# Kernel optimization log

Hardware: AMD Instinct MI355X
Metric: run time of the kernel (lower is better)

The kernel has to match this reference:

```python
import jax, jax.numpy as jnp
import numpy as np
from jax import lax

B, L, E, P, K, KS, H, T = 64, 512, 256, 64, 512, 3, 512, 53
V, MAXL = 50000, 512


def _span_idx(k):
    ks, kl = jax.random.split(k)
    starts = jax.random.randint(ks, (B,), 1, L - 9)
    spans = jax.random.randint(kl, (B,), 0, 8)
    return jnp.stack([starts, starts + spans], axis=1)  # [B,2], 1<=s<=e<L-1


def setup_inputs() -> dict:
    key = jax.random.key(0)
    ks = jax.random.split(key, 12)
    context = jax.random.randint(ks[0], (B, L), 0, V)
    subject_idx = _span_idx(ks[1])
    object_idx = _span_idx(ks[2])
    subject_dis = jax.random.randint(ks[3], (B, L), 0, 2 * MAXL)
    object_dis = jax.random.randint(ks[4], (B, L), 0, 2 * MAXL)
    embed_table = jax.random.normal(ks[5], (V, E), jnp.float32) * 0.02
    pos_table = jax.random.normal(ks[6], (2 * MAXL, P), jnp.float32) * 0.02
    Cin = 3 * E + 2 * P
    conv_w = jax.random.normal(ks[7], (K, Cin, KS), jnp.float32) * 0.02
    conv_b = jnp.zeros((K,), jnp.float32)
    lin1_w = jax.random.normal(ks[8], (H, K), jnp.float32) * 0.02
    lin1_b = jnp.zeros((H,), jnp.float32)
    lin2_w = jax.random.normal(ks[9], (T, 6 * E + H), jnp.float32) * 0.02
    lin2_b = jnp.zeros((T,), jnp.float32)
    return {"context": context, "subject_idx": subject_idx, "object_idx": object_idx,
            "subject_dis": subject_dis, "object_dis": object_dis,
            "embed_table": embed_table, "pos_table": pos_table,
            "conv_w": conv_w, "conv_b": conv_b,
            "lin1_w": lin1_w, "lin1_b": lin1_b, "lin2_w": lin2_w, "lin2_b": lin2_b}


def _entity_features(embed, idx):
    # embed: [B,L,E'], idx: [B,2] (start,end) inclusive span
    s, e = idx[:, 0], idx[:, 1]
    pos = jnp.arange(L)
    mask = (pos[None, :] >= s[:, None]) & (pos[None, :] <= e[:, None])  # [B,L]
    cnt = mask.sum(axis=1).astype(embed.dtype)[:, None]
    mean = jnp.einsum('ble,bl->be', embed, mask.astype(embed.dtype)) / cnt
    bidx = jnp.arange(embed.shape[0])
    left = embed[bidx, s - 1]                       # start>=1 always in data (torch: start>=0 branch)
    right_ok = (e + 1) < L
    right = jnp.where(right_ok[:, None], embed[bidx, jnp.clip(e + 1, 0, L - 1)], 0.0)
    return jnp.concatenate([mean, left, right], axis=1)  # [B,3E']


def reference(context, subject_idx, object_idx, subject_dis, object_dis,
              embed_table, pos_table, conv_w, conv_b,
              lin1_w, lin1_b, lin2_w, lin2_b):
    embed = embed_table[context]                    # [B,L,E]
    subj = _entity_features(embed, subject_idx)     # [B,3E]
    obj = _entity_features(embed, object_idx)       # [B,3E]

    # shift-and-concat window features (zero pad one step each side)
    epad = jnp.pad(embed, ((0, 0), (1, 1), (0, 0)))
    word = jnp.concatenate([epad[:, :-2], epad[:, 1:-1], epad[:, 2:]], axis=2)  # [B,L,3E]

    pos_feat = jnp.concatenate([pos_table[subject_dis], pos_table[object_dis]], axis=2)  # [B,L,2P]
    sent = jnp.concatenate([word, pos_feat], axis=2).transpose(0, 2, 1)  # [B,C,L]

    conv = lax.conv_general_dilated(sent, conv_w, window_strides=(1,),
                                    padding=[(KS // 2, KS // 2)],
                                    dimension_numbers=('NCH', 'OIH', 'NCH'))
    conv = conv + conv_b[None, :, None]             # [B,K,L]
    pooled = conv.max(axis=2)                       # global maxpool -> [B,K]
    sent_h = jnp.tanh(pooled @ lin1_w.T + lin1_b)   # [B,H]

    com = jnp.concatenate([subj, obj, sent_h], axis=1)  # [B,6E+H]
    scores = com @ lin2_w.T + lin2_b                # [B,T]; decode = argmax(scores, 1)
    return scores
```

## Files before the change

kernel.cpp:

```cpp
#include <hip/hip_runtime.h>
#include <hip/hip_bf16.h>
#include <hip/hip_fp8.h>
#include <stdint.h>

#define B_   64
#define L_   512
#define E_   256
#define P_   64
#define KOUT 512
#define KS_  3
#define H_   512
#define T_   53
#define CINW 2688
#define LE   516
#define LPP  514
#define COMW 2048

#define FP8_S    64.0f
#define DESCALE  (1.0f / 4096.0f)

#define SEC_CW    0
#define SEC_EMBP  512
#define SEC_POSP  (SEC_EMBP + (B_ * LE / 4))
#define SEC_ENT   (SEC_POSP + (B_ * LPP / 4))
#define SEC_POOL  (SEC_ENT + 2 * B_)
#define SEC_END   (SEC_POOL + 32)

typedef __attribute__((ext_vector_type(4))) float f32x4;
typedef __attribute__((ext_vector_type(4))) int   i32x4;
typedef __attribute__((ext_vector_type(8))) int   i32x8;

__device__ __forceinline__ unsigned enc_f(float x) {
    unsigned u = __float_as_uint(x);
    return (u & 0x80000000u) ? ~u : (u | 0x80000000u);
}
__device__ __forceinline__ float dec_f(unsigned e) {
    return __uint_as_float((e & 0x80000000u) ? (e & 0x7fffffffu) : ~e);
}
__device__ __forceinline__ unsigned char f8c(float x) {
    __hip_fp8_e4m3 t(x);
    return t.__x;
}

__device__ __forceinline__ void cp16(const void* g, void* l) {
    __builtin_amdgcn_global_load_lds(
        (const __attribute__((address_space(1))) unsigned int*)g,
        (__attribute__((address_space(3))) unsigned int*)l,
        16, 0, 0);
}

__global__ void prep(const float* __restrict__ conv_w,
                     const int* __restrict__ context,
                     const int* __restrict__ sidx,
                     const int* __restrict__ oidx,
                     const int* __restrict__ sdis,
                     const int* __restrict__ odis,
                     const float* __restrict__ etab,
                     const float* __restrict__ ptab,
                     unsigned char* __restrict__ wce,
                     unsigned char* __restrict__ wcp,
                     __hip_bfloat16* __restrict__ wcorr,
                     unsigned char* __restrict__ embp,
                     unsigned char* __restrict__ posp,
                     float* __restrict__ com,
                     unsigned* __restrict__ pooled) {
    __shared__ float w[CINW];
    const int blk = blockIdx.x;
    const int tid = threadIdx.x;

    if (blk < SEC_EMBP) {
        int n = blk;
        const float* src = conv_w + (size_t)n * CINW;
        for (int i = tid; i < CINW; i += 256) w[i] = src[i];
        __syncthreads();
        for (int i = tid; i < 5 * E_; i += 256) {
            int d = i >> 8, c = i & 255;
            float s = 0.f;
#pragma unroll
            for (int tau = 0; tau <= 2; tau++) {
                int seg = d - tau;
                if (seg >= 0 && seg <= 2) s += w[(seg * 256 + c) * 3 + tau];
            }
            wce[((size_t)d * KOUT + n) * E_ + c] = f8c(s * FP8_S);
        }
        for (int i = tid; i < 3 * 128; i += 256) {
            int tau = i >> 7, p = i & 127;
            wcp[((size_t)tau * KOUT + n) * 128 + p] = f8c(w[(768 + p) * 3 + tau] * FP8_S);
        }
        for (int i = tid; i < 2 * E_; i += 256) {
            int which = i >> 8, c = i & 255;
            wcorr[((size_t)which * KOUT + n) * E_ + c] =
                __float2bfloat16(which ? w[c * 3 + 2] : w[(512 + c) * 3 + 0]);
        }
    } else if (blk < SEC_POSP) {
        int row = (blk - SEC_EMBP) * 4 + (tid >> 6);
        int lane = tid & 63;
        int b = row / LE, r = row % LE;
        unsigned char* out = embp + (size_t)row * E_;
        if (r < 2 || r >= LE - 2) {
            *(uchar4*)(out + lane * 4) = (uchar4){0, 0, 0, 0};
            return;
        }
        int token = context[b * L_ + (r - 2)];
        float4 v = *(const float4*)(etab + (size_t)token * E_ + lane * 4);
        uchar4 pk;
        pk.x = f8c(v.x * FP8_S); pk.y = f8c(v.y * FP8_S);
        pk.z = f8c(v.z * FP8_S); pk.w = f8c(v.w * FP8_S);
        *(uchar4*)(out + lane * 4) = pk;
    } else if (blk < SEC_ENT) {
        int row = (blk - SEC_POSP) * 4 + (tid >> 6);
        int lane = tid & 63;
        int b = row / LPP, r = row % LPP;
        unsigned char* out = posp + (size_t)row * 128;
        if (r < 1 || r >= LPP - 1) {
            *(unsigned short*)(out + lane * 2) = 0;
            return;
        }
        int l = r - 1;
        int which = lane >> 5;
        int i2 = (lane & 31) * 2;
        int t = which ? odis[b * L_ + l] : sdis[b * L_ + l];
        float2 v = *(const float2*)(ptab + (size_t)t * P_ + i2);
        unsigned short pk = (unsigned short)f8c(v.x * FP8_S)
                          | ((unsigned short)f8c(v.y * FP8_S) << 8);
        *(unsigned short*)(out + which * 64 + i2) = pk;
    } else if (blk < SEC_POOL) {
        int idx = blk - SEC_ENT;
        int b = idx >> 1, which = idx & 1;
        const int* sp = which ? oidx : sidx;
        int s = sp[b * 2 + 0], e = sp[b * 2 + 1];
        const int* ctx = context + b * L_;
        float* outb = com + (size_t)b * COMW + which * 768;
        int d = tid;
        float sum = 0.f;
        for (int x = s; x <= e; ++x) sum += etab[(size_t)ctx[x] * E_ + d];
        outb[d] = sum / (float)(e - s + 1);
        outb[256 + d] = etab[(size_t)ctx[s - 1] * E_ + d];
        float r = 0.f;
        if (e + 1 < L_) r = etab[(size_t)ctx[e + 1] * E_ + d];
        outb[512 + d] = r;
    } else {
        int base = ((blk - SEC_POOL) * 256 + tid) * 4;
        *(uint4*)(pooled + base) = (uint4){0, 0, 0, 0};
    }
}

__global__ void corr_k(const int* __restrict__ ctx,
                       const float* __restrict__ etab,
                       const __hip_bfloat16* __restrict__ wcorr,
                       float* __restrict__ corr) {
    int wid = blockIdx.x * 4 + (threadIdx.x >> 6);
    int lane = threadIdx.x & 63;
    int n4    = wid & 127;
    int which = (wid >> 7) & 1;
    int b     = wid >> 8;
    int token = ctx[b * L_ + (which ? L_ - 1 : 0)];
    float4 ev = *(const float4*)(etab + (size_t)token * E_ + lane * 4);
#pragma unroll
    for (int k = 0; k < 4; k++) {
        int n = n4 * 4 + k;
        const __hip_bfloat16* wr = wcorr + ((size_t)which * KOUT + n) * E_ + lane * 4;
        float s = ev.x * __bfloat162float(wr[0]) + ev.y * __bfloat162float(wr[1])
                + ev.z * __bfloat162float(wr[2]) + ev.w * __bfloat162float(wr[3]);
#pragma unroll
        for (int off = 32; off > 0; off >>= 1) s += __shfl_down(s, off, 64);
        if (lane == 0) corr[(b * 2 + which) * KOUT + n] = s;
    }
}

__global__ void __launch_bounds__(256, 2)
conv_gemm_pool(const unsigned char* __restrict__ embp,
               const unsigned char* __restrict__ posp,
               const unsigned char* __restrict__ wce,
               const unsigned char* __restrict__ wcp,
               const float* __restrict__ corr,
               unsigned* __restrict__ pooled) {
    __shared__ unsigned char sT[2][2][128 * 128];

    const int tid  = threadIdx.x;
    const int lane = tid & 63;
    const int wave = tid >> 6;
    const int mt = blockIdx.x;
    const int nt = blockIdx.y;
    const int b  = mt >> 2;
    const int l0 = (mt & 3) * 128;
    const int n0 = nt * 128;

    const int wr = (wave & 1) * 64;
    const int wc = (wave >> 1) * 64;
    const int m  = lane & 15;
    const int q  = lane >> 4;

    f32x4 acc[4][4];
#pragma unroll
    for (int i = 0; i < 4; i++)
#pragma unroll
        for (int j = 0; j < 4; j++) acc[i][j] = (f32x4){0.f, 0.f, 0.f, 0.f};

    const int srow = tid >> 3;
    const int ssw  = ((tid & 7) ^ (srow & 7)) << 4;

    auto bases = [&](int t, const char*& A, int& As, const char*& Bx, int& Bs) {
        if (t < 10) {
            int tap = t >> 1, kc = (t & 1) << 7;
            A  = (const char*)embp + ((size_t)(b * LE + l0 + tap) << 8) + kc;
            As = E_;
            Bx = (const char*)wce + ((size_t)(tap * KOUT + n0) << 8) + kc;
            Bs = E_;
        } else {
            int tap = t - 10;
            A  = (const char*)posp + ((size_t)(b * LPP + l0 + tap) << 7);
            As = 128;
            Bx = (const char*)wcp + ((size_t)(tap * KOUT + n0) << 7);
            Bs = 128;
        }
    };

    auto stage = [&](int bf_, const char* A, int As, const char* Bx, int Bs) {
        char* dA = (char*)&sT[bf_][0][0] + tid * 16;
        char* dB = (char*)&sT[bf_][1][0] + tid * 16;
#pragma unroll
        for (int rnd = 0; rnd < 4; rnd++) {
            int r = srow + rnd * 32;
            cp16(A  + r * As + ssw, dA + rnd * 4096);
            cp16(Bx + r * Bs + ssw, dB + rnd * 4096);
        }
    };

    auto frag = [&](const unsigned char* base, int row) -> i32x8 {
        const unsigned char* rp = base + row * 128;
        int x  = (row & 7) << 4;
        i32x4 lo = *(const i32x4*)(rp + (((q << 1) << 4) ^ x));
        i32x4 hi = *(const i32x4*)(rp + ((((q << 1) | 1) << 4) ^ x));
        return (i32x8){lo[0], lo[1], lo[2], lo[3], hi[0], hi[1], hi[2], hi[3]};
    };

    auto compute = [&](int bf_) {
        const unsigned char* pA = &sT[bf_][0][0];
        const unsigned char* pB = &sT[bf_][1][0];
        i32x8 af[4];
#pragma unroll
        for (int i = 0; i < 4; i++) af[i] = frag(pA, wr + i * 16 + m);
#pragma unroll
        for (int j = 0; j < 4; j++) {
            i32x8 bfv = frag(pB, wc + j * 16 + m);
#pragma unroll
            for (int i = 0; i < 4; i++)
                acc[i][j] = __builtin_amdgcn_mfma_scale_f32_16x16x128_f8f6f4(
                    af[i], bfv, acc[i][j], 0, 0, 0, 0x7f7f7f7f, 0, 0x7f7f7f7f);
        }
    };

    {
        const char *A0, *B0; int As0, Bs0;
        bases(0, A0, As0, B0, Bs0);
        stage(0, A0, As0, B0, Bs0);
    }
    int cur = 0;
#pragma unroll 1
    for (int t = 0; t < 13; t++) {
        if (t < 12) {
            const char *A1, *B1; int As1, Bs1;
            bases(t + 1, A1, As1, B1, Bs1);
            stage(cur ^ 1, A1, As1, B1, Bs1);
            asm volatile("s_waitcnt vmcnt(8)" ::: "memory");
        } else {
            asm volatile("s_waitcnt vmcnt(0)" ::: "memory");
        }
        __builtin_amdgcn_s_barrier();
        __builtin_amdgcn_sched_barrier(0);
        compute(cur);
        __builtin_amdgcn_sched_barrier(0);
        __builtin_amdgcn_s_barrier();
        cur ^= 1;
    }

    const float* corrb = corr + b * 2 * KOUT;
#pragma unroll
    for (int j = 0; j < 4; j++) {
        int col = n0 + wc + j * 16 + m;
        float mx = -3.4e38f;
#pragma unroll
        for (int i = 0; i < 4; i++)
#pragma unroll
            for (int r = 0; r < 4; r++) {
                float v = acc[i][j][r] * DESCALE;
                int l = l0 + wr + i * 16 + q * 4 + r;
                if (l == 0)      v -= corrb[col];
                if (l == L_ - 1) v -= corrb[KOUT + col];
                mx = fmaxf(mx, v);
            }
        mx = fmaxf(mx, __shfl_xor(mx, 16, 64));
        mx = fmaxf(mx, __shfl_xor(mx, 32, 64));
        if (q == 0) atomicMax(&pooled[b * KOUT + col], enc_f(mx));
    }
}

__global__ void lin1_k(const unsigned* __restrict__ pooled,
                       const float* __restrict__ conv_b,
                       const float* __restrict__ lin1_w,
                       const float* __restrict__ lin1_b,
                       float* __restrict__ com) {
    int bid = blockIdx.x;
    int wave = threadIdx.x >> 6, lane = threadIdx.x & 63;
    int b = bid >> 7;
    int h = (bid & 127) * 4 + wave;
    const float* w = lin1_w + (size_t)h * KOUT;
    const unsigned* pb = pooled + b * KOUT;
    float s = 0.f;
#pragma unroll
    for (int i = 0; i < 8; i++) {
        int k = lane + 64 * i;
        s += (dec_f(pb[k]) + conv_b[k]) * w[k];
    }
#pragma unroll
    for (int off = 32; off > 0; off >>= 1) s += __shfl_down(s, off, 64);
    if (lane == 0) com[(size_t)b * COMW + 1536 + h] = tanhf(s + lin1_b[h]);
}

__global__ void lin2_k(const float* __restrict__ com,
                       const float* __restrict__ lin2_w,
                       const float* __restrict__ lin2_b,
                       float* __restrict__ out) {
    int b = blockIdx.x;
    int wave = threadIdx.x >> 6, lane = threadIdx.x & 63;
    int t = blockIdx.y * 4 + wave;
    if (t >= T_) return;
    const float* w = lin2_w + (size_t)t * COMW;
    const float* c = com + (size_t)b * COMW;
    float s = 0.f;
#pragma unroll
    for (int i = 0; i < 32; i++) {
        int k = lane + 64 * i;
        s += c[k] * w[k];
    }
#pragma unroll
    for (int off = 32; off > 0; off >>= 1) s += __shfl_down(s, off, 64);
    if (lane == 0) out[b * T_ + t] = s + lin2_b[t];
}

extern "C" void kernel_launch(void* const* d_in, const int* in_sizes, int n_in,
                              void* d_out, int out_size, void* d_ws, size_t ws_size,
                              hipStream_t stream) {
    const int*   context = (const int*)d_in[0];
    const int*   sidx    = (const int*)d_in[1];
    const int*   oidx    = (const int*)d_in[2];
    const int*   sdis    = (const int*)d_in[3];
    const int*   odis    = (const int*)d_in[4];
    const float* etab    = (const float*)d_in[5];
    const float* ptab    = (const float*)d_in[6];
    const float* conv_w  = (const float*)d_in[7];
    const float* conv_b  = (const float*)d_in[8];
    const float* lin1_w  = (const float*)d_in[9];
    const float* lin1_b  = (const float*)d_in[10];
    const float* lin2_w  = (const float*)d_in[11];
    const float* lin2_b  = (const float*)d_in[12];
    float* out = (float*)d_out;

    char* ws = (char*)d_ws;
    size_t off = 0;
    unsigned char* embp = (unsigned char*)(ws + off);
    off += (size_t)B_ * LE * E_;
    off = (off + 255) & ~(size_t)255;
    unsigned char* posp = (unsigned char*)(ws + off);
    off += (size_t)B_ * LPP * 128;
    off = (off + 255) & ~(size_t)255;
    unsigned char* wce = (unsigned char*)(ws + off);
    off += (size_t)5 * KOUT * E_;
    off = (off + 255) & ~(size_t)255;
    unsigned char* wcp = (unsigned char*)(ws + off);
    off += (size_t)3 * KOUT * 128;
    off = (off + 255) & ~(size_t)255;
    __hip_bfloat16* wcorr = (__hip_bfloat16*)(ws + off);
    off += (size_t)2 * KOUT * E_ * 2;
    off = (off + 255) & ~(size_t)255;
    float* corr = (float*)(ws + off);
    off += (size_t)B_ * 2 * KOUT * 4;
    off = (off + 255) & ~(size_t)255;
    unsigned* pooled = (unsigned*)(ws + off);
    off += (size_t)B_ * KOUT * 4;
    off = (off + 255) & ~(size_t)255;
    float* com = (float*)(ws + off);
    off += (size_t)B_ * COMW * 4;

    prep<<<dim3(SEC_END), dim3(256), 0, stream>>>(
        conv_w, context, sidx, oidx, sdis, odis, etab, ptab,
        wce, wcp, wcorr, embp, posp, com, pooled);
    corr_k<<<dim3(4096), dim3(256), 0, stream>>>(context, etab, wcorr, corr);
    conv_gemm_pool<<<dim3(256, 4), dim3(256), 0, stream>>>(embp, posp, wce, wcp, corr, pooled);
    lin1_k<<<dim3(8192), dim3(256), 0, stream>>>(pooled, conv_b, lin1_w, lin1_b, com);
    lin2_k<<<dim3(B_, 14), dim3(256), 0, stream>>>(com, lin2_w, lin2_b, out);
}
```

Baseline: 181.4 us.

## Reuse one A window across conv taps and fold corr into prep

```diff
diff --git a/kernel.cpp b/kernel.cpp
--- a/kernel.cpp
+++ b/kernel.cpp
@@ -59,9 +59,9 @@
                      const float* __restrict__ ptab,
                      unsigned char* __restrict__ wce,
                      unsigned char* __restrict__ wcp,
-                     __hip_bfloat16* __restrict__ wcorr,
                      unsigned char* __restrict__ embp,
                      unsigned char* __restrict__ posp,
+                     float* __restrict__ corr,
                      float* __restrict__ com,
                      unsigned* __restrict__ pooled) {
     __shared__ float w[CINW];
@@ -87,10 +87,22 @@
             int tau = i >> 7, p = i & 127;
             wcp[((size_t)tau * KOUT + n) * 128 + p] = f8c(w[(768 + p) * 3 + tau] * FP8_S);
         }
-        for (int i = tid; i < 2 * E_; i += 256) {
-            int which = i >> 8, c = i & 255;
-            wcorr[((size_t)which * KOUT + n) * E_ + c] =
-                __float2bfloat16(which ? w[c * 3 + 2] : w[(512 + c) * 3 + 0]);
+        {
+            int p   = tid >> 1, sub = tid & 1;
+            int bb  = p >> 1, which = p & 1;
+            int token = context[bb * L_ + (which ? L_ - 1 : 0)];
+            const float4* er4 = (const float4*)(etab + (size_t)token * E_ + sub * 128);
+            int A = which ? (sub * 384 + 2) : (1536 + sub * 384);
+            float s = 0.f;
+#pragma unroll 8
+            for (int c4 = 0; c4 < 32; c4++) {
+                float4 v = er4[c4];
+                int c = c4 * 4;
+                s += v.x * w[A + 3 * c]     + v.y * w[A + 3 * c + 3]
+                   + v.z * w[A + 3 * c + 6] + v.w * w[A + 3 * c + 9];
+            }
+            s += __shfl_xor(s, 1, 64);
+            if (sub == 0) corr[(bb * 2 + which) * KOUT + n] = s;
         }
     } else if (blk < SEC_POSP) {
         int row = (blk - SEC_EMBP) * 4 + (tid >> 6);
@@ -145,37 +157,15 @@
     }
 }
 
-__global__ void corr_k(const int* __restrict__ ctx,
-                       const float* __restrict__ etab,
-                       const __hip_bfloat16* __restrict__ wcorr,
-                       float* __restrict__ corr) {
-    int wid = blockIdx.x * 4 + (threadIdx.x >> 6);
-    int lane = threadIdx.x & 63;
-    int n4    = wid & 127;
-    int which = (wid >> 7) & 1;
-    int b     = wid >> 8;
-    int token = ctx[b * L_ + (which ? L_ - 1 : 0)];
-    float4 ev = *(const float4*)(etab + (size_t)token * E_ + lane * 4);
-#pragma unroll
-    for (int k = 0; k < 4; k++) {
-        int n = n4 * 4 + k;
-        const __hip_bfloat16* wr = wcorr + ((size_t)which * KOUT + n) * E_ + lane * 4;
-        float s = ev.x * __bfloat162float(wr[0]) + ev.y * __bfloat162float(wr[1])
-                + ev.z * __bfloat162float(wr[2]) + ev.w * __bfloat162float(wr[3]);
-#pragma unroll
-        for (int off = 32; off > 0; off >>= 1) s += __shfl_down(s, off, 64);
-        if (lane == 0) corr[(b * 2 + which) * KOUT + n] = s;
-    }
-}
-
-__global__ void __launch_bounds__(256, 2)
+__global__ void __launch_bounds__(256, 3)
 conv_gemm_pool(const unsigned char* __restrict__ embp,
                const unsigned char* __restrict__ posp,
                const unsigned char* __restrict__ wce,
                const unsigned char* __restrict__ wcp,
                const float* __restrict__ corr,
                unsigned* __restrict__ pooled) {
-    __shared__ unsigned char sT[2][2][128 * 128];
+    __shared__ unsigned char winA[136 * 128];
+    __shared__ unsigned char sB[2][128 * 128];
 
     const int tid  = threadIdx.x;
     const int lane = tid & 63;
@@ -199,51 +189,53 @@
 
     const int srow = tid >> 3;
     const int ssw  = ((tid & 7) ^ (srow & 7)) << 4;
-
-    auto bases = [&](int t, const char*& A, int& As, const char*& Bx, int& Bs) {
+    auto stageB = [&](int buf, int t) {
+        const unsigned char* base; int stride;
         if (t < 10) {
-            int tap = t >> 1, kc = (t & 1) << 7;
-            A  = (const char*)embp + ((size_t)(b * LE + l0 + tap) << 8) + kc;
-            As = E_;
-            Bx = (const char*)wce + ((size_t)(tap * KOUT + n0) << 8) + kc;
-            Bs = E_;
+            int tap = (t < 5) ? t : t - 5;
+            int kc  = (t < 5) ? 0 : 128;
+            base = wce + (size_t)(tap * KOUT + n0) * E_ + kc;
+            stride = E_;
         } else {
             int tap = t - 10;
-            A  = (const char*)posp + ((size_t)(b * LPP + l0 + tap) << 7);
-            As = 128;
-            Bx = (const char*)wcp + ((size_t)(tap * KOUT + n0) << 7);
-            Bs = 128;
-        }
+            base = wcp + (size_t)(tap * KOUT + n0) * 128;
+            stride = 128;
+        }
+        char* dB = (char*)sB[buf] + tid * 16;
+#pragma unroll
+        for (int rnd = 0; rnd < 4; rnd++)
+            cp16(base + (srow + rnd * 32) * stride + ssw, dB + rnd * 4096);
     };
 
-    auto stage = [&](int bf_, const char* A, int As, const char* Bx, int Bs) {
-        char* dA = (char*)&sT[bf_][0][0] + tid * 16;
-        char* dB = (char*)&sT[bf_][1][0] + tid * 16;
-#pragma unroll
-        for (int rnd = 0; rnd < 4; rnd++) {
-            int r = srow + rnd * 32;
-            cp16(A  + r * As + ssw, dA + rnd * 4096);
-            cp16(Bx + r * Bs + ssw, dB + rnd * 4096);
+    auto stageWin = [&](const unsigned char* base, int stride) {
+#pragma unroll
+        for (int k = 0; k < 4; k++) {
+            int idx = tid + k * 256;
+            int r = idx >> 3, c = idx & 7;
+            cp16(base + r * stride + ((c ^ (r & 7)) << 4), (char*)winA + idx * 16);
+        }
+        if (tid < 64) {
+            int idx = tid + 1024;
+            int r = idx >> 3, c = idx & 7;
+            cp16(base + r * stride + ((c ^ (r & 7)) << 4), (char*)winA + idx * 16);
         }
     };
 
-    auto frag = [&](const unsigned char* base, int row) -> i32x8 {
-        const unsigned char* rp = base + row * 128;
-        int x  = (row & 7) << 4;
+    auto frag = [&](const unsigned char* rowbase, int row) -> i32x8 {
+        const unsigned char* rp = rowbase + row * 128;
+        int x = (row & 7) << 4;
         i32x4 lo = *(const i32x4*)(rp + (((q << 1) << 4) ^ x));
         i32x4 hi = *(const i32x4*)(rp + ((((q << 1) | 1) << 4) ^ x));
         return (i32x8){lo[0], lo[1], lo[2], lo[3], hi[0], hi[1], hi[2], hi[3]};
     };
 
-    auto compute = [&](int bf_) {
-        const unsigned char* pA = &sT[bf_][0][0];
-        const unsigned char* pB = &sT[bf_][1][0];
+    auto compute = [&](int buf, int tap) {
         i32x8 af[4];
 #pragma unroll
-        for (int i = 0; i < 4; i++) af[i] = frag(pA, wr + i * 16 + m);
+        for (int i = 0; i < 4; i++) af[i] = frag(winA, tap + wr + i * 16 + m);
 #pragma unroll
         for (int j = 0; j < 4; j++) {
-            i32x8 bfv = frag(pB, wc + j * 16 + m);
+            i32x8 bfv = frag(sB[buf], wc + j * 16 + m);
 #pragma unroll
             for (int i = 0; i < 4; i++)
                 acc[i][j] = __builtin_amdgcn_mfma_scale_f32_16x16x128_f8f6f4(
@@ -251,27 +243,33 @@
         }
     };
 
-    {
-        const char *A0, *B0; int As0, Bs0;
-        bases(0, A0, As0, B0, Bs0);
-        stage(0, A0, As0, B0, Bs0);
-    }
+    stageWin(embp + (size_t)(b * LE + l0) * E_, E_);
+    stageB(0, 0);
+    asm volatile("s_waitcnt vmcnt(0)" ::: "memory");
+    __builtin_amdgcn_s_barrier();
+
     int cur = 0;
 #pragma unroll 1
     for (int t = 0; t < 13; t++) {
-        if (t < 12) {
-            const char *A1, *B1; int As1, Bs1;
-            bases(t + 1, A1, As1, B1, Bs1);
-            stage(cur ^ 1, A1, As1, B1, Bs1);
-            asm volatile("s_waitcnt vmcnt(8)" ::: "memory");
+        bool pend = (t == 4 || t == 9);
+        if (t < 12 && !pend) {
+            stageB(cur ^ 1, t + 1);
+            asm volatile("s_waitcnt vmcnt(4)" ::: "memory");
         } else {
             asm volatile("s_waitcnt vmcnt(0)" ::: "memory");
         }
         __builtin_amdgcn_s_barrier();
         __builtin_amdgcn_sched_barrier(0);
-        compute(cur);
+        compute(cur, (t < 5) ? t : (t < 10 ? t - 5 : t - 10));
         __builtin_amdgcn_sched_barrier(0);
         __builtin_amdgcn_s_barrier();
+        if (pend) {
+            if (t == 4) stageWin(embp + (size_t)(b * LE + l0) * E_ + 128, E_);
+            else        stageWin(posp + (size_t)(b * LPP + l0) * 128, 128);
+            stageB(cur ^ 1, t + 1);
+            asm volatile("s_waitcnt vmcnt(0)" ::: "memory");
+            __builtin_amdgcn_s_barrier();
+        }
         cur ^= 1;
     }
 
@@ -371,9 +369,6 @@
     unsigned char* wcp = (unsigned char*)(ws + off);
     off += (size_t)3 * KOUT * 128;
     off = (off + 255) & ~(size_t)255;
-    __hip_bfloat16* wcorr = (__hip_bfloat16*)(ws + off);
-    off += (size_t)2 * KOUT * E_ * 2;
-    off = (off + 255) & ~(size_t)255;
     float* corr = (float*)(ws + off);
     off += (size_t)B_ * 2 * KOUT * 4;
     off = (off + 255) & ~(size_t)255;
@@ -385,8 +380,7 @@
 
     prep<<<dim3(SEC_END), dim3(256), 0, stream>>>(
         conv_w, context, sidx, oidx, sdis, odis, etab, ptab,
-        wce, wcp, wcorr, embp, posp, com, pooled);
-    corr_k<<<dim3(4096), dim3(256), 0, stream>>>(context, etab, wcorr, corr);
+        wce, wcp, embp, posp, corr, com, pooled);
     conv_gemm_pool<<<dim3(256, 4), dim3(256), 0, stream>>>(embp, posp, wce, wcp, corr, pooled);
     lin1_k<<<dim3(8192), dim3(256), 0, stream>>>(pooled, conv_b, lin1_w, lin1_b, com);
     lin2_k<<<dim3(B_, 14), dim3(256), 0, stream>>>(com, lin2_w, lin2_b, out);
```

Measured after the change: 184.9 us. Within noise of the previous version (+1.9%).

## Fold boundary-correction into prep and fuse lin1/lin2 into one kernel

Applied to the files above, without the earlier changes.

```diff
diff --git a/kernel.cpp b/kernel.cpp
--- a/kernel.cpp
+++ b/kernel.cpp
@@ -59,9 +59,9 @@
                      const float* __restrict__ ptab,
                      unsigned char* __restrict__ wce,
                      unsigned char* __restrict__ wcp,
-                     __hip_bfloat16* __restrict__ wcorr,
                      unsigned char* __restrict__ embp,
                      unsigned char* __restrict__ posp,
+                     float* __restrict__ corr,
                      float* __restrict__ com,
                      unsigned* __restrict__ pooled) {
     __shared__ float w[CINW];
@@ -87,10 +87,22 @@
             int tau = i >> 7, p = i & 127;
             wcp[((size_t)tau * KOUT + n) * 128 + p] = f8c(w[(768 + p) * 3 + tau] * FP8_S);
         }
-        for (int i = tid; i < 2 * E_; i += 256) {
-            int which = i >> 8, c = i & 255;
-            wcorr[((size_t)which * KOUT + n) * E_ + c] =
-                __float2bfloat16(which ? w[c * 3 + 2] : w[(512 + c) * 3 + 0]);
+        {
+            int p   = tid >> 1, sub = tid & 1;
+            int bb  = p >> 1, which = p & 1;
+            int token = context[bb * L_ + (which ? L_ - 1 : 0)];
+            const float4* er4 = (const float4*)(etab + (size_t)token * E_ + sub * 128);
+            int A = which ? (sub * 384 + 2) : (1536 + sub * 384);
+            float s = 0.f;
+#pragma unroll 8
+            for (int c4 = 0; c4 < 32; c4++) {
+                float4 v = er4[c4];
+                int c = c4 * 4;
+                s += v.x * w[A + 3 * c]     + v.y * w[A + 3 * c + 3]
+                   + v.z * w[A + 3 * c + 6] + v.w * w[A + 3 * c + 9];
+            }
+            s += __shfl_xor(s, 1, 64);
+            if (sub == 0) corr[(bb * 2 + which) * KOUT + n] = s;
         }
     } else if (blk < SEC_POSP) {
         int row = (blk - SEC_EMBP) * 4 + (tid >> 6);
@@ -145,29 +157,6 @@
     }
 }
 
-__global__ void corr_k(const int* __restrict__ ctx,
-                       const float* __restrict__ etab,
-                       const __hip_bfloat16* __restrict__ wcorr,
-                       float* __restrict__ corr) {
-    int wid = blockIdx.x * 4 + (threadIdx.x >> 6);
-    int lane = threadIdx.x & 63;
-    int n4    = wid & 127;
-    int which = (wid >> 7) & 1;
-    int b     = wid >> 8;
-    int token = ctx[b * L_ + (which ? L_ - 1 : 0)];
-    float4 ev = *(const float4*)(etab + (size_t)token * E_ + lane * 4);
-#pragma unroll
-    for (int k = 0; k < 4; k++) {
-        int n = n4 * 4 + k;
-        const __hip_bfloat16* wr = wcorr + ((size_t)which * KOUT + n) * E_ + lane * 4;
-        float s = ev.x * __bfloat162float(wr[0]) + ev.y * __bfloat162float(wr[1])
-                + ev.z * __bfloat162float(wr[2]) + ev.w * __bfloat162float(wr[3]);
-#pragma unroll
-        for (int off = 32; off > 0; off >>= 1) s += __shfl_down(s, off, 64);
-        if (lane == 0) corr[(b * 2 + which) * KOUT + n] = s;
-    }
-}
-
 __global__ void __launch_bounds__(256, 2)
 conv_gemm_pool(const unsigned char* __restrict__ embp,
                const unsigned char* __restrict__ posp,
@@ -296,47 +285,58 @@
     }
 }
 
-__global__ void lin1_k(const unsigned* __restrict__ pooled,
-                       const float* __restrict__ conv_b,
-                       const float* __restrict__ lin1_w,
-                       const float* __restrict__ lin1_b,
-                       float* __restrict__ com) {
-    int bid = blockIdx.x;
-    int wave = threadIdx.x >> 6, lane = threadIdx.x & 63;
-    int b = bid >> 7;
-    int h = (bid & 127) * 4 + wave;
-    const float* w = lin1_w + (size_t)h * KOUT;
-    const unsigned* pb = pooled + b * KOUT;
-    float s = 0.f;
-#pragma unroll
-    for (int i = 0; i < 8; i++) {
-        int k = lane + 64 * i;
-        s += (dec_f(pb[k]) + conv_b[k]) * w[k];
-    }
-#pragma unroll
-    for (int off = 32; off > 0; off >>= 1) s += __shfl_down(s, off, 64);
-    if (lane == 0) com[(size_t)b * COMW + 1536 + h] = tanhf(s + lin1_b[h]);
-}
-
-__global__ void lin2_k(const float* __restrict__ com,
-                       const float* __restrict__ lin2_w,
-                       const float* __restrict__ lin2_b,
-                       float* __restrict__ out) {
-    int b = blockIdx.x;
-    int wave = threadIdx.x >> 6, lane = threadIdx.x & 63;
-    int t = blockIdx.y * 4 + wave;
-    if (t >= T_) return;
-    const float* w = lin2_w + (size_t)t * COMW;
+__global__ void lin_fused(const unsigned* __restrict__ pooled,
+                          const float* __restrict__ conv_b,
+                          const float* __restrict__ lin1_w,
+                          const float* __restrict__ lin1_b,
+                          const float* __restrict__ com,
+                          const float* __restrict__ lin2_w,
+                          const float* __restrict__ lin2_b,
+                          float* __restrict__ out) {
+    __shared__ float padj[KOUT];
+    __shared__ float sh[H_];
+    const int b    = blockIdx.x;
+    const int tid  = threadIdx.x;
+    const int wave = tid >> 6, lane = tid & 63;
+
+    if (tid < KOUT) padj[tid] = dec_f(pooled[b * KOUT + tid]) + conv_b[tid];
+    __syncthreads();
+
+#pragma unroll 1
+    for (int hh = 0; hh < 32; ++hh) {
+        int h = wave * 32 + hh;
+        const float* w = lin1_w + (size_t)h * KOUT;
+        float s = 0.f;
+#pragma unroll
+        for (int i = 0; i < 8; i++) {
+            int k = lane + 64 * i;
+            s += padj[k] * w[k];
+        }
+#pragma unroll
+        for (int off = 32; off > 0; off >>= 1) s += __shfl_down(s, off, 64);
+        if (lane == 0) sh[h] = tanhf(s + lin1_b[h]);
+    }
+    __syncthreads();
+
     const float* c = com + (size_t)b * COMW;
-    float s = 0.f;
-#pragma unroll
-    for (int i = 0; i < 32; i++) {
-        int k = lane + 64 * i;
-        s += c[k] * w[k];
-    }
-#pragma unroll
-    for (int off = 32; off > 0; off >>= 1) s += __shfl_down(s, off, 64);
-    if (lane == 0) out[b * T_ + t] = s + lin2_b[t];
+#pragma unroll 1
+    for (int t = wave; t < T_; t += 16) {
+        const float* w = lin2_w + (size_t)t * COMW;
+        float s = 0.f;
+#pragma unroll
+        for (int i = 0; i < 24; i++) {
+            int j = lane + 64 * i;
+            s += c[j] * w[j];
+        }
+#pragma unroll
+        for (int i = 24; i < 32; i++) {
+            int j = lane + 64 * i;
+            s += sh[j - 1536] * w[j];
+        }
+#pragma unroll
+        for (int off = 32; off > 0; off >>= 1) s += __shfl_down(s, off, 64);
+        if (lane == 0) out[b * T_ + t] = s + lin2_b[t];
+    }
 }
 
 extern "C" void kernel_launch(void* const* d_in, const int* in_sizes, int n_in,
@@ -371,9 +371,6 @@
     unsigned char* wcp = (unsigned char*)(ws + off);
     off += (size_t)3 * KOUT * 128;
     off = (off + 255) & ~(size_t)255;
-    __hip_bfloat16* wcorr = (__hip_bfloat16*)(ws + off);
-    off += (size_t)2 * KOUT * E_ * 2;
-    off = (off + 255) & ~(size_t)255;
     float* corr = (float*)(ws + off);
     off += (size_t)B_ * 2 * KOUT * 4;
     off = (off + 255) & ~(size_t)255;
@@ -385,9 +382,8 @@
 
     prep<<<dim3(SEC_END), dim3(256), 0, stream>>>(
         conv_w, context, sidx, oidx, sdis, odis, etab, ptab,
-        wce, wcp, wcorr, embp, posp, com, pooled);
-    corr_k<<<dim3(4096), dim3(256), 0, stream>>>(context, etab, wcorr, corr);
+        wce, wcp, embp, posp, corr, com, pooled);
     conv_gemm_pool<<<dim3(256, 4), dim3(256), 0, stream>>>(embp, posp, wce, wcp, corr, pooled);
-    lin1_k<<<dim3(8192), dim3(256), 0, stream>>>(pooled, conv_b, lin1_w, lin1_b, com);
-    lin2_k<<<dim3(B_, 14), dim3(256), 0, stream>>>(com, lin2_w, lin2_b, out);
-}
+    lin_fused<<<dim3(B_), dim3(1024), 0, stream>>>(
+        pooled, conv_b, lin1_w, lin1_b, com, lin2_w, lin2_b, out);
+}
```

New measurement: 190.3 us. 4.9% more time.
